# Kernel optimization log

Hardware: AMD Instinct MI355X
Metric: run time of the kernel (lower is better)

The kernel has to match this reference:

```python
import math
import jax, jax.numpy as jnp
import numpy as np

B, L, D, H = 8, 4096, 512, 8
FACTOR = 1


def setup_inputs() -> dict:
    key = jax.random.key(0)
    ks = jax.random.split(key, 8)
    scale = 0.02
    return {
        "queries": jax.random.normal(ks[0], (B, L, D), dtype=jnp.float32),
        "keys": jax.random.normal(ks[1], (B, L, D), dtype=jnp.float32),
        "values": jax.random.normal(ks[2], (B, L, D), dtype=jnp.float32),
        "Wq": jax.random.normal(ks[3], (D, D), dtype=jnp.float32) * scale,
        "bq": jnp.zeros((D,), dtype=jnp.float32),
        "Wk": jax.random.normal(ks[4], (D, D), dtype=jnp.float32) * scale,
        "bk": jnp.zeros((D,), dtype=jnp.float32),
        "Wv": jax.random.normal(ks[5], (D, D), dtype=jnp.float32) * scale,
        "bv": jnp.zeros((D,), dtype=jnp.float32),
        "Wo": jax.random.normal(ks[6], (D, D), dtype=jnp.float32) * scale,
        "bo": jnp.zeros((D,), dtype=jnp.float32),
    }


def reference(queries, keys, values, Wq, bq, Wk, bk, Wv, bv, Wo, bo):
    b, l, d = queries.shape
    h = H
    e = d // h
    # Projections (torch Linear math; weight stored as [in, out] here)
    q = (queries @ Wq + bq).reshape(b, l, h, e)
    k = (keys @ Wk + bk).reshape(b, l, h, e)
    v = (values @ Wv + bv).reshape(b, l, h, e)
    # [B, H, E, L]
    qp = q.transpose(0, 2, 3, 1)
    kp = k.transpose(0, 2, 3, 1)
    vp = v.transpose(0, 2, 3, 1)
    # FFT cross-correlation over the time axis
    qf = jnp.fft.rfft(qp, axis=-1)
    kf = jnp.fft.rfft(kp, axis=-1)
    corr = jnp.fft.irfft(qf * jnp.conj(kf), n=l, axis=-1)  # [B,H,E,L]
    # time_delay_agg_training
    top_k = int(FACTOR * math.log(l))
    mean_value = corr.mean(axis=(1, 2))  # [B, L] (mean over head then channel)
    _, index = jax.lax.top_k(mean_value.mean(axis=0), top_k)  # [K] shared delays
    weights = mean_value[:, index]  # [B, K]
    tmp_corr = jax.nn.softmax(weights, axis=-1)  # [B, K]
    # roll(values, -delay) along time == gather at (t + delay) mod L
    idx = (jnp.arange(l)[None, :] + index[:, None]) % l  # [K, L]
    gathered = jnp.take(vp, idx, axis=-1)  # [B, H, E, K, L]
    agg = jnp.einsum("bhekl,bk->bhel", gathered, tmp_corr)  # weighted MAC over delays
    out = agg.transpose(0, 3, 1, 2).reshape(b, l, h * e)  # [B, L, D]
    return out @ Wo + bo
```

## Files before the change

kernel.cpp:

```cpp
#include <hip/hip_runtime.h>
#include <math.h>

#define LSEQ 4096
#define DMODEL 512
#define BB 8
#define TOPK 8
#define ML (BB * LSEQ)
#define FFT_CH 2
#define NGRP (DMODEL / FFT_CH)
#define PPH 2052

typedef unsigned short u16;
typedef unsigned int u32;
typedef float f32x4 __attribute__((ext_vector_type(4)));
typedef short s16x8 __attribute__((ext_vector_type(8)));
typedef u16 u16x8 __attribute__((ext_vector_type(8)));

__device__ __forceinline__ u16 rne_bf16(float f) {
    u32 u = __float_as_uint(f);
    return (u16)((u + 0x7FFF + ((u >> 16) & 1)) >> 16);
}

__device__ __forceinline__ void fft16(float (&zr)[16], float (&zi)[16]) {
    const float C1 = 0.92387953251128674f, S1 = 0.38268343236508978f, R2 = 0.70710678118654752f;
#define BF0(i, j) { float ar=zr[i],ai=zi[i],br=zr[j],bi=zi[j]; zr[i]=ar+br; zi[i]=ai+bi; zr[j]=ar-br; zi[j]=ai-bi; }
#define BFW(i, j, wr, wi) { float ar=zr[i],ai=zi[i],br=zr[j],bi=zi[j]; zr[i]=ar+br; zi[i]=ai+bi; float dr=ar-br, di=ai-bi; zr[j]=dr*(wr)-di*(wi); zi[j]=dr*(wi)+di*(wr); }
#define BFI(i, j) { float ar=zr[i],ai=zi[i],br=zr[j],bi=zi[j]; zr[i]=ar+br; zi[i]=ai+bi; float dr=ar-br, di=ai-bi; zr[j]=di; zi[j]=-dr; }
    BF0(0, 8); BFW(1, 9, C1, -S1); BFW(2, 10, R2, -R2); BFW(3, 11, S1, -C1);
    BFI(4, 12); BFW(5, 13, -S1, -C1); BFW(6, 14, -R2, -R2); BFW(7, 15, -C1, -S1);
    BF0(0, 4); BFW(1, 5, R2, -R2); BFI(2, 6); BFW(3, 7, -R2, -R2);
    BF0(8, 12); BFW(9, 13, R2, -R2); BFI(10, 14); BFW(11, 15, -R2, -R2);
    BF0(0, 2); BFI(1, 3); BF0(4, 6); BFI(5, 7);
    BF0(8, 10); BFI(9, 11); BF0(12, 14); BFI(13, 15);
    BF0(0, 1); BF0(2, 3); BF0(4, 5); BF0(6, 7);
    BF0(8, 9); BF0(10, 11); BF0(12, 13); BF0(14, 15);
#undef BF0
#undef BFW
#undef BFI
}

template <bool WRITEBACK>
__device__ __forceinline__ void fft4096_r16_core(float* __restrict__ lre, float* __restrict__ lim, int t,
                                                 float (&ozr)[16], float (&ozi)[16]) {
    constexpr int REV16[16] = {0, 8, 4, 12, 2, 10, 6, 14, 1, 9, 5, 13, 3, 11, 7, 15};
    float zr[16], zi[16];
#pragma unroll
    for (int gg = 0; gg < 16; ++gg) {
        int n = 256 * gg + t;
        int p = n ^ ((gg & 3) << 2) ^ ((gg & 1) << 4);
        zr[gg] = lre[p]; zi[gg] = lim[p];
    }
    fft16(zr, zi);
    {
        const int n1 = t >> 4;
        float w1i, w1r;
        __sincosf(-0.0245436926061702596f * (float)n1, &w1i, &w1r);
        float wr = 1.f, wi = 0.f;
#pragma unroll
        for (int k0 = 0; k0 < 16; ++k0) {
            float vr = zr[REV16[k0]], vi = zi[REV16[k0]];
            if (k0) {
                float nr = wr * w1r - wi * w1i;
                wi = wr * w1i + wi * w1r;
                wr = nr;
                float tr = vr * wr - vi * wi;
                vi = vr * wi + vi * wr;
                vr = tr;
            }
            int n = 256 * k0 + t;
            int p = n ^ ((k0 & 3) << 2) ^ ((k0 & 1) << 4);
            lre[p] = vr; lim[p] = vi;
        }
    }
    __syncthreads();
    {
        const int k0 = t >> 4, n2 = t & 15;
        const int x0 = ((k0 & 3) << 2) | ((k0 & 1) << 4);
#pragma unroll
        for (int gg = 0; gg < 16; ++gg) {
            int n = 256 * k0 + 16 * gg + n2;
            zr[gg] = lre[n ^ x0]; zi[gg] = lim[n ^ x0];
        }
        fft16(zr, zi);
        float wbi, wbr, wsi, wsr;
        __sincosf(-0.00153398078788564123f * (float)(n2 * k0), &wbi, &wbr);
        __sincosf(-0.0245436926061702596f * (float)n2, &wsi, &wsr);
        float wr = wbr, wi = wbi;
#pragma unroll
        for (int k1 = 0; k1 < 16; ++k1) {
            float vr = zr[REV16[k1]], vi = zi[REV16[k1]];
            if (k1) {
                float nr = wr * wsr - wi * wsi;
                wi = wr * wsi + wi * wsr;
                wr = nr;
            }
            float tr = vr * wr - vi * wi;
            vi = vr * wi + vi * wr;
            vr = tr;
            int n = 256 * k0 + 16 * k1 + n2;
            lre[n ^ x0] = vr; lim[n ^ x0] = vi;
        }
    }
    __syncthreads();
    {
        const int k0 = t & 15, k1 = t >> 4;
        const int nb4 = 64 * k0 + 4 * k1;
        const int xv = (k0 & 3) | ((k0 & 1) << 2);
#pragma unroll
        for (int i = 0; i < 4; ++i) {
            int p4 = (nb4 + i) ^ xv;
            float4 fr = *(const float4*)&lre[4 * p4];
            float4 fi = *(const float4*)&lim[4 * p4];
            ozr[4 * i + 0] = fr.x; ozr[4 * i + 1] = fr.y; ozr[4 * i + 2] = fr.z; ozr[4 * i + 3] = fr.w;
            ozi[4 * i + 0] = fi.x; ozi[4 * i + 1] = fi.y; ozi[4 * i + 2] = fi.z; ozi[4 * i + 3] = fi.w;
        }
        fft16(ozr, ozi);
        if constexpr (WRITEBACK) {
            __syncthreads();
#pragma unroll
            for (int r = 0; r < 16; ++r) {
                const int k2 = REV16[r];
                lre[t + 256 * k2] = ozr[r];
                lim[t + 256 * k2] = ozi[r];
            }
            __syncthreads();
        }
    }
}

__global__ __launch_bounds__(256) void fft_cross(const u16* __restrict__ Qtb,
                                                 const u16* __restrict__ Ktb,
                                                 float* __restrict__ Ppart) {
    __shared__ float lre[4096];
    __shared__ float lim[4096];
    constexpr int REV16[16] = {0, 8, 4, 12, 2, 10, 6, 14, 1, 9, 5, 13, 3, 11, 7, 15};
    const int t = threadIdx.x;
    const int b = blockIdx.x / NGRP;
    const int g = blockIdx.x % NGRP;

    float2 acc[8];
#pragma unroll
    for (int i = 0; i < 8; ++i) acc[i] = make_float2(0.f, 0.f);
    float accn = 0.f;

    const uint4* q8 = (const uint4*)(Qtb + (size_t)(g * FFT_CH) * ML + (size_t)b * LSEQ);
    const uint4* k8 = (const uint4*)(Ktb + (size_t)(g * FFT_CH) * ML + (size_t)b * LSEQ);

    uint4 pq[2], pk[2];
    pq[0] = q8[t]; pq[1] = q8[t + 256];
    pk[0] = k8[t]; pk[1] = k8[t + 256];

    for (int c = 0; c < FFT_CH; ++c) {
        __syncthreads();
#pragma unroll
        for (int i = 0; i < 2; ++i) {
            const int u = t + 256 * i;
            const uint4 vq = pq[i], vk = pk[i];
#pragma unroll
            for (int hh = 0; hh < 2; ++hh) {
                const int v = 2 * u + hh;
                const int key = (v >> 6) & 15;
                const int p4 = v ^ (key & 3) ^ ((key & 1) << 2);
                const u32 w0 = hh ? vq.z : vq.x;
                const u32 w1 = hh ? vq.w : vq.y;
                float4 fa = make_float4(__uint_as_float(w0 << 16), __uint_as_float(w0 & 0xFFFF0000u),
                                        __uint_as_float(w1 << 16), __uint_as_float(w1 & 0xFFFF0000u));
                *(float4*)&lre[4 * p4] = fa;
                const u32 x0 = hh ? vk.z : vk.x;
                const u32 x1 = hh ? vk.w : vk.y;
                float4 fb = make_float4(__uint_as_float(x0 << 16), __uint_as_float(x0 & 0xFFFF0000u),
                                        __uint_as_float(x1 << 16), __uint_as_float(x1 & 0xFFFF0000u));
                *(float4*)&lim[4 * p4] = fb;
            }
        }
        if (c + 1 < FFT_CH) {
            const uint4* qn = q8 + (size_t)(c + 1) * (ML / 8);
            const uint4* kn = k8 + (size_t)(c + 1) * (ML / 8);
            pq[0] = qn[t]; pq[1] = qn[t + 256];
            pk[0] = kn[t]; pk[1] = kn[t + 256];
        }
        __syncthreads();
        float ozr[16], ozi[16];
        fft4096_r16_core<true>(lre, lim, t, ozr, ozi);
#pragma unroll
        for (int i = 0; i < 8; ++i) {
            const int j = i * 256 + t;
            const int nj = (4096 - j) & 4095;
            const int r = REV16[i];
            float zfr = ozr[r], zfi = ozi[r];
            float znr = lre[nj], zni = lim[nj];
            float qr = 0.5f * (zfr + znr);
            float qi = 0.5f * (zfi - zni);
            float kr = 0.5f * (zfi + zni);
            float ki = -0.5f * (zfr - znr);
            acc[i].x += qr * kr + qi * ki;
            acc[i].y += qi * kr - qr * ki;
        }
        if (t == 0) accn += ozr[1] * ozi[1];
    }
    float2* Pp = (float2*)Ppart + (size_t)blockIdx.x * PPH;
#pragma unroll
    for (int i = 0; i < 8; ++i) Pp[i * 256 + t] = acc[i];
    if (t == 0) Pp[2048] = make_float2(accn, 0.f);
}

__device__ __forceinline__ void gemmQ_body(const float* __restrict__ A,
                                           const u16* __restrict__ Bhi,
                                           u16* __restrict__ Ct, int lin, int tid,
                                           u16* sAhi, u16* sBhi) {
    const int t = (lin & 7) * 128 + (lin >> 3);
    const int bm = (t >> 2) * 128;
    const int bn = (t & 3) * 128;
    const int lane = tid & 63, wid = tid >> 6;
    const int wm = wid >> 1, wn = wid & 1;
    const int l15 = lane & 15, kg = lane >> 4;

    f32x4 acc[4][4] = {};

    for (int k0 = 0; k0 < 512; k0 += 64) {
        __syncthreads();
#pragma unroll
        for (int it = 0; it < 4; ++it) {
            const int ch = it * 256 + tid;
            const int row = ch >> 3, c = ch & 7;
            const float* ga = A + (size_t)(bm + row) * 512 + k0 + c * 8;
            float4 f0 = *(const float4*)ga;
            float4 f1 = *(const float4*)(ga + 4);
            float fs[8] = {f0.x, f0.y, f0.z, f0.w, f1.x, f1.y, f1.z, f1.w};
            u32 h[4];
#pragma unroll
            for (int p = 0; p < 4; ++p) {
                u32 u0 = __float_as_uint(fs[2 * p]);
                u32 u1 = __float_as_uint(fs[2 * p + 1]);
                u32 h0 = u0 + 0x7FFF + ((u0 >> 16) & 1);
                u32 h1 = u1 + 0x7FFF + ((u1 >> 16) & 1);
                h[p] = __builtin_amdgcn_perm(h1, h0, 0x07060302u);
            }
            const int off = row * 64 + ((c ^ (row & 7)) << 3);
            *(uint4*)&sAhi[off] = make_uint4(h[0], h[1], h[2], h[3]);
        }
#pragma unroll
        for (int it = 0; it < 4; ++it) {
            const int ch = it * 256 + tid;
            const int row = ch >> 3, c = ch & 7;
            const int off = row * 64 + ((c ^ (row & 7)) << 3);
            const size_t gg = (size_t)(bn + row) * 512 + k0 + c * 8;
            *(u16x8*)&sBhi[off] = *(const u16x8*)&Bhi[gg];
        }
        __syncthreads();
#pragma unroll
        for (int kk = 0; kk < 2; ++kk) {
            const int cbase = kk * 4 + kg;
            s16x8 ah[4], bh[4];
#pragma unroll
            for (int mi = 0; mi < 4; ++mi) {
                const int row = wm * 64 + mi * 16 + l15;
                const int off = row * 64 + (((cbase ^ (row & 7))) << 3);
                ah[mi] = *(const s16x8*)&sAhi[off];
            }
#pragma unroll
            for (int ni = 0; ni < 4; ++ni) {
                const int row = wn * 64 + ni * 16 + l15;
                const int off = row * 64 + (((cbase ^ (row & 7))) << 3);
                bh[ni] = *(const s16x8*)&sBhi[off];
            }
#pragma unroll
            for (int ni = 0; ni < 4; ++ni)
#pragma unroll
                for (int mi = 0; mi < 4; ++mi)
                    acc[mi][ni] = __builtin_amdgcn_mfma_f32_16x16x32_bf16(ah[mi], bh[ni], acc[mi][ni], 0, 0, 0);
        }
    }
#pragma unroll
    for (int ni = 0; ni < 4; ++ni) {
        const int d = bn + wn * 64 + ni * 16 + l15;
#pragma unroll
        for (int mi = 0; mi < 4; ++mi) {
            const int rb = bm + wm * 64 + mi * 16 + (kg << 2);
            ushort4 o;
            o.x = rne_bf16(acc[mi][ni][0]); o.y = rne_bf16(acc[mi][ni][1]);
            o.z = rne_bf16(acc[mi][ni][2]); o.w = rne_bf16(acc[mi][ni][3]);
            *(ushort4*)&Ct[(size_t)d * ML + rb] = o;
        }
    }
}

__device__ __forceinline__ void gemm1_body(const float* __restrict__ A,
                                           const u16* __restrict__ Bhi,
                                           const float* __restrict__ bias,
                                           u16* __restrict__ Cv, int lin, int tid,
                                           u16* sAhi, u16* sBhi) {
    const int t = (lin & 7) * 128 + (lin >> 3);
    const int bm = (t >> 2) * 128;
    const int bn = (t & 3) * 128;
    const int lane = tid & 63, wid = tid >> 6;
    const int wm = wid >> 1, wn = wid & 1;
    const int l15 = lane & 15, kg = lane >> 4;

    f32x4 acc[4][4] = {};

    for (int k0 = 0; k0 < 512; k0 += 64) {
        __syncthreads();
#pragma unroll
        for (int it = 0; it < 4; ++it) {
            const int ch = it * 256 + tid;
            const int row = ch >> 3, c = ch & 7;
            const float* ga = A + (size_t)(bm + row) * 512 + k0 + c * 8;
            float4 f0 = *(const float4*)ga;
            float4 f1 = *(const float4*)(ga + 4);
            float fs[8] = {f0.x, f0.y, f0.z, f0.w, f1.x, f1.y, f1.z, f1.w};
            u32 h[4];
#pragma unroll
            for (int p = 0; p < 4; ++p) {
                u32 u0 = __float_as_uint(fs[2 * p]);
                u32 u1 = __float_as_uint(fs[2 * p + 1]);
                u32 h0 = u0 + 0x7FFF + ((u0 >> 16) & 1);
                u32 h1 = u1 + 0x7FFF + ((u1 >> 16) & 1);
                h[p] = __builtin_amdgcn_perm(h1, h0, 0x07060302u);
            }
            const int off = row * 64 + ((c ^ (row & 7)) << 3);
            *(uint4*)&sAhi[off] = make_uint4(h[0], h[1], h[2], h[3]);
        }
#pragma unroll
        for (int it = 0; it < 4; ++it) {
            const int ch = it * 256 + tid;
            const int row = ch >> 3, c = ch & 7;
            const int off = row * 64 + ((c ^ (row & 7)) << 3);
            const size_t gg = (size_t)(bn + row) * 512 + k0 + c * 8;
            *(u16x8*)&sBhi[off] = *(const u16x8*)&Bhi[gg];
        }
        __syncthreads();
#pragma unroll
        for (int kk = 0; kk < 2; ++kk) {
            const int cbase = kk * 4 + kg;
            s16x8 ah[4], bh[4];
#pragma unroll
            for (int mi = 0; mi < 4; ++mi) {
                const int row = wm * 64 + mi * 16 + l15;
                const int off = row * 64 + (((cbase ^ (row & 7))) << 3);
                ah[mi] = *(const s16x8*)&sAhi[off];
            }
#pragma unroll
            for (int ni = 0; ni < 4; ++ni) {
                const int row = wn * 64 + ni * 16 + l15;
                const int off = row * 64 + (((cbase ^ (row & 7))) << 3);
                bh[ni] = *(const s16x8*)&sBhi[off];
            }
#pragma unroll
            for (int ni = 0; ni < 4; ++ni)
#pragma unroll
                for (int mi = 0; mi < 4; ++mi)
                    acc[mi][ni] = __builtin_amdgcn_mfma_f32_16x16x32_bf16(ah[mi], bh[ni], acc[mi][ni], 0, 0, 0);
        }
    }
#pragma unroll
    for (int ni = 0; ni < 4; ++ni) {
        const int col = bn + wn * 64 + ni * 16 + l15;
        const float bvv = bias[col];
#pragma unroll
        for (int mi = 0; mi < 4; ++mi) {
            const int rb = bm + wm * 64 + mi * 16 + (kg << 2);
#pragma unroll
            for (int r = 0; r < 4; ++r)
                Cv[(size_t)(rb + r) * 512 + col] = rne_bf16(acc[mi][ni][r] + bvv);
        }
    }
}

__global__ __launch_bounds__(256) void prep_all(const float* __restrict__ Wq, const float* __restrict__ Wk,
                                                const float* __restrict__ Wv, const float* __restrict__ Wo,
                                                const float* __restrict__ bvec, const float* __restrict__ bo,
                                                u16* __restrict__ Mh, u16* __restrict__ Wch,
                                                float* __restrict__ bc) {
    __shared__ float As[16][64];
    __shared__ float Ws[16][64];
    __shared__ float red[8][32];
    const int bx = blockIdx.x;
    const int tid = threadIdx.x;
    if (bx < 128) {
        const bool isM = bx < 64;
        const int id = bx & 63;
        const int bm = (id >> 3) * 64, bn = (id & 7) * 64;
        const int tx = tid & 15, ty = tid >> 4;
        float acc[4][4] = {};
        const int arow = tid >> 2, ak4 = tid & 3;
        const int wrow = tid >> 4, wc4 = tid & 15;
        const float* Abase = isM ? Wq : Wv;
        for (int k0 = 0; k0 < 512; k0 += 16) {
            float4 av = *(const float4*)&Abase[(size_t)(bm + arow) * 512 + k0 + ak4 * 4];
            float4 wv4;
            if (isM) wv4 = *(const float4*)&Wk[(size_t)(bn + arow) * 512 + k0 + ak4 * 4];
            else     wv4 = *(const float4*)&Wo[(size_t)(k0 + wrow) * 512 + bn + wc4 * 4];
            __syncthreads();
            As[ak4 * 4 + 0][arow] = av.x;
            As[ak4 * 4 + 1][arow] = av.y;
            As[ak4 * 4 + 2][arow] = av.z;
            As[ak4 * 4 + 3][arow] = av.w;
            if (isM) {
                Ws[ak4 * 4 + 0][arow] = wv4.x;
                Ws[ak4 * 4 + 1][arow] = wv4.y;
                Ws[ak4 * 4 + 2][arow] = wv4.z;
                Ws[ak4 * 4 + 3][arow] = wv4.w;
            } else {
                *(float4*)&Ws[wrow][wc4 * 4] = wv4;
            }
            __syncthreads();
#pragma unroll
            for (int k = 0; k < 16; ++k) {
                float4 a = *(const float4*)&As[k][ty * 4];
                float4 b = *(const float4*)&Ws[k][tx * 4];
                acc[0][0] += a.x * b.x; acc[0][1] += a.x * b.y; acc[0][2] += a.x * b.z; acc[0][3] += a.x * b.w;
                acc[1][0] += a.y * b.x; acc[1][1] += a.y * b.y; acc[1][2] += a.y * b.z; acc[1][3] += a.y * b.w;
                acc[2][0] += a.z * b.x; acc[2][1] += a.z * b.y; acc[2][2] += a.z * b.z; acc[2][3] += a.z * b.w;
                acc[3][0] += a.w * b.x; acc[3][1] += a.w * b.y; acc[3][2] += a.w * b.z; acc[3][3] += a.w * b.w;
            }
        }
        u16* dh = isM ? Mh : Wch;
#pragma unroll
        for (int i = 0; i < 4; ++i)
#pragma unroll
            for (int j = 0; j < 4; ++j) {
                const int a = bm + ty * 4 + i;
                const int n = bn + tx * 4 + j;
                dh[(size_t)n * 512 + a] = rne_bf16(acc[i][j]);
            }
    } else {
        const int n0 = (bx - 128) * 32;
        const int nl = tid & 31, jg = tid >> 5;
        float partial = 0.f;
        for (int s = 0; s < 64; ++s) {
            int j = jg + 8 * s;
            partial += bvec[j] * Wo[(size_t)j * 512 + n0 + nl];
        }
        red[jg][nl] = partial;
        __syncthreads();
        if (tid < 32) {
            float s2 = 0.f;
            for (int r2 = 0; r2 < 8; ++r2) s2 += red[r2][tid];
            bc[n0 + tid] = s2 + bo[n0 + tid];
        }
    }
}

__global__ __launch_bounds__(256, 4) void proj3(const float* __restrict__ queries,
                                                const u16* __restrict__ Mh, u16* __restrict__ Qtb,
                                                const float* __restrict__ values,
                                                const u16* __restrict__ Wch, const float* __restrict__ bc,
                                                u16* __restrict__ VOb,
                                                const float* __restrict__ keys, u16* __restrict__ Ktb) {
    __shared__ __align__(16) u16 smem[2 * 128 * 64];
    const int g = blockIdx.x;
    const int q = g / 6, r = g % 6;
    const int tid = threadIdx.x;
    if (r == 0) {
        gemmQ_body(queries, Mh, Qtb, q, tid, smem, smem + 8192);
    } else if (r == 1) {
        gemm1_body(values, Wch, bc, VOb, q, tid, smem, smem + 8192);
    } else {
        float* Ts = (float*)smem;
        const int tb = q * 4 + (r - 2);
        const int bd = (tb & 7) * 64;
        const int bm = (tb >> 3) * 64;
        const int rr = tid >> 2, c4 = tid & 3;
#pragma unroll
        for (int i = 0; i < 4; ++i) {
            const int c0 = (c4 + 4 * i) * 4;
            float4 v = *(const float4*)&keys[(size_t)(bm + rr) * DMODEL + bd + c0];
            Ts[rr * 65 + c0 + 0] = v.x; Ts[rr * 65 + c0 + 1] = v.y;
            Ts[rr * 65 + c0 + 2] = v.z; Ts[rr * 65 + c0 + 3] = v.w;
        }
        __syncthreads();
        const int dl = tid >> 2, m4 = tid & 3;
#pragma unroll
        for (int i = 0; i < 4; ++i) {
            const int m0 = (m4 + 4 * i) * 4;
            ushort4 o;
            o.x = rne_bf16(Ts[(m0 + 0) * 65 + dl]);
            o.y = rne_bf16(Ts[(m0 + 1) * 65 + dl]);
            o.z = rne_bf16(Ts[(m0 + 2) * 65 + dl]);
            o.w = rne_bf16(Ts[(m0 + 3) * 65 + dl]);
            *(ushort4*)&Ktb[(size_t)(bd + dl) * ML + bm + m0] = o;
        }
    }
}

__global__ __launch_bounds__(256) void reduce_ppart(const float2* __restrict__ Pp,
                                                    float2* __restrict__ Pred) {
    const int j = blockIdx.x * 256 + threadIdx.x;
    const int b = blockIdx.y;
    if (j > 2048) return;
    float sr = 0.f, si = 0.f;
    const float2* base = Pp + (size_t)b * NGRP * PPH + j;
    for (int g = 0; g < NGRP; ++g) {
        float2 p = base[(size_t)g * PPH];
        sr += p.x;
        si += p.y;
    }
    Pred[(size_t)b * PPH + j] = make_float2(sr, si);
}

__global__ __launch_bounds__(256) void ifft_mean(const float2* __restrict__ Pred,
                                                 float* __restrict__ mv) {
    __shared__ float lre[4096];
    __shared__ float lim[4096];
    constexpr int REV16[16] = {0, 8, 4, 12, 2, 10, 6, 14, 1, 9, 5, 13, 3, 11, 7, 15};
    const int t = threadIdx.x;
    const int b = blockIdx.x;
    for (int j = t; j < 4096; j += 256) {
        float2 p;
        if (j <= 2048) {
            p = Pred[(size_t)b * PPH + j];
        } else {
            p = Pred[(size_t)b * PPH + (4096 - j)];
            p.y = -p.y;
        }
        int key = (j >> 8) & 15;
        int ph = j ^ ((key & 3) << 2) ^ ((key & 1) << 4);
        lre[ph] = p.x;
        lim[ph] = -p.y;
    }
    __syncthreads();
    float ozr[16], ozi[16];
    fft4096_r16_core<false>(lre, lim, t, ozr, ozi);
    const float scale = 1.0f / (4096.0f * 512.0f);
#pragma unroll
    for (int i = 0; i < 16; ++i)
        mv[(size_t)b * 4096 + t + 256 * i] = ozr[REV16[i]] * scale;
}

__global__ __launch_bounds__(1024) void topk_softmax(const float* __restrict__ mv,
                                                     int* __restrict__ idxO,
                                                     float* __restrict__ tcO) {
    __shared__ float vals[4096];
    __shared__ float wv[16];
    __shared__ int wix[16];
    __shared__ int sidx[TOPK];
    const int tid = threadIdx.x;
    const int lane = tid & 63, wvid = tid >> 6;
    for (int j = tid; j < 4096; j += 1024) {
        float s = 0.f;
        for (int b = 0; b < BB; ++b) s += mv[(size_t)b * 4096 + j];
        vals[j] = s * 0.125f;
    }
    __syncthreads();
    for (int k = 0; k < TOPK; ++k) {
        float best = -INFINITY;
        int bi = 0x7fffffff;
        for (int j = tid; j < 4096; j += 1024) {
            float v = vals[j];
            if (v > best) { best = v; bi = j; }
        }
#pragma unroll
        for (int off = 32; off > 0; off >>= 1) {
            float ov = __shfl_down(best, off);
            int oi = __shfl_down(bi, off);
            if (ov > best || (ov == best && oi < bi)) { best = ov; bi = oi; }
        }
        if (lane == 0) { wv[wvid] = best; wix[wvid] = bi; }
        __syncthreads();
        if (wvid == 0) {
            best = (lane < 16) ? wv[lane] : -INFINITY;
            bi = (lane < 16) ? wix[lane] : 0x7fffffff;
#pragma unroll
            for (int off = 8; off > 0; off >>= 1) {
                float ov = __shfl_down(best, off);
                int oi = __shfl_down(bi, off);
                if (ov > best || (ov == best && oi < bi)) { best = ov; bi = oi; }
            }
            if (lane == 0) {
                sidx[k] = bi;
                idxO[k] = bi;
                vals[bi] = -INFINITY;
            }
        }
        __syncthreads();
    }
    if (tid < BB) {
        float w[TOPK];
        float m = -INFINITY;
        for (int k = 0; k < TOPK; ++k) {
            w[k] = mv[(size_t)tid * 4096 + sidx[k]];
            m = fmaxf(m, w[k]);
        }
        float s = 0.f;
        for (int k = 0; k < TOPK; ++k) { w[k] = expf(w[k] - m); s += w[k]; }
        float inv = 1.0f / s;
        for (int k = 0; k < TOPK; ++k) tcO[tid * TOPK + k] = w[k] * inv;
    }
}

__global__ __launch_bounds__(256) void gather_out(const u16* __restrict__ VO,
                                                  const int* __restrict__ idx,
                                                  const float* __restrict__ tc,
                                                  float* __restrict__ out) {
    const int e = blockIdx.x * 256 + threadIdx.x;
    const int d8 = e & 63;
    const int l = (e >> 6) & 4095;
    const int b = e >> 18;
    float s[8] = {};
#pragma unroll
    for (int k = 0; k < TOPK; ++k) {
        const int src = (l + idx[k]) & 4095;
        const float w = tc[b * TOPK + k];
        uint4 v = *(const uint4*)&VO[((size_t)(b * 4096 + src)) * 512 + d8 * 8];
        s[0] += w * __uint_as_float(v.x << 16);
        s[1] += w * __uint_as_float(v.x & 0xFFFF0000u);
        s[2] += w * __uint_as_float(v.y << 16);
        s[3] += w * __uint_as_float(v.y & 0xFFFF0000u);
        s[4] += w * __uint_as_float(v.z << 16);
        s[5] += w * __uint_as_float(v.z & 0xFFFF0000u);
        s[6] += w * __uint_as_float(v.w << 16);
        s[7] += w * __uint_as_float(v.w & 0xFFFF0000u);
    }
    const size_t ob = ((size_t)(b * 4096 + l)) * 512 + d8 * 8;
    *(float4*)&out[ob]     = make_float4(s[0], s[1], s[2], s[3]);
    *(float4*)&out[ob + 4] = make_float4(s[4], s[5], s[6], s[7]);
}

extern "C" void kernel_launch(void* const* d_in, const int* in_sizes, int n_in,
                              void* d_out, int out_size, void* d_ws, size_t ws_size,
                              hipStream_t stream) {
    const float* queries = (const float*)d_in[0];
    const float* keys    = (const float*)d_in[1];
    const float* values  = (const float*)d_in[2];
    const float* Wq = (const float*)d_in[3];
    const float* Wk = (const float*)d_in[5];
    const float* Wv = (const float*)d_in[7];
    const float* bv = (const float*)d_in[8];
    const float* Wo = (const float*)d_in[9];
    const float* bo = (const float*)d_in[10];
    float* out = (float*)d_out;

    const size_t SZ = (size_t)ML * DMODEL;
    u16* Qtb = (u16*)d_ws;
    u16* Ktb = Qtb + SZ;
    u16* VOb = Ktb + SZ;
    float* Pp   = (float*)(VOb + SZ);
    float* Pred = Pp + (size_t)BB * NGRP * PPH * 2;
    float* mv   = Pred + (size_t)BB * PPH * 2;
    int*   idx  = (int*)(mv + 32768);
    float* tc   = mv + 32768 + 16;
    float* bc   = mv + 32768 + 96;
    u16* Mh  = (u16*)(bc + 512);
    u16* Wch = Mh + 262144;

    dim3 blk(256);

    prep_all<<<dim3(144), blk, 0, stream>>>(Wq, Wk, Wv, Wo, bv, bo, Mh, Wch, bc);

    proj3<<<dim3(6144), blk, 0, stream>>>(queries, Mh, Qtb, values, Wch, bc, VOb, keys, Ktb);

    fft_cross<<<dim3(BB * NGRP), blk, 0, stream>>>(Qtb, Ktb, Pp);

    reduce_ppart<<<dim3(9, BB), blk, 0, stream>>>((const float2*)Pp, (float2*)Pred);

    ifft_mean<<<dim3(BB), blk, 0, stream>>>((const float2*)Pred, mv);

    topk_softmax<<<dim3(1), dim3(1024), 0, stream>>>(mv, idx, tc);

    gather_out<<<dim3((BB * LSEQ * (DMODEL / 8)) / 256), blk, 0, stream>>>(VOb, idx, tc, out);
}
```

Before: 276.3 us.

## Prefetch GEMM tiles into registers, reorder proj3 blocks, split partial reduction

Both GEMM bodies now load the next K-slice of A and B into registers while the current slice is being computed, a form of software pipelining. This hides global memory latency at the cost of more registers, and the launch-bounds occupancy hint of 4 blocks is dropped. proj3 now assigns contiguous block ranges to the Q GEMM, the V GEMM and the K transpose instead of interleaving them by g%6. reduce_ppart is split four ways along the group axis to expose more parallelism, with ifft_mean summing the four partial results.

```diff
diff --git a/kernel.cpp b/kernel.cpp
--- a/kernel.cpp
+++ b/kernel.cpp
@@ -214,6 +214,19 @@
     const int lane = tid & 63, wid = tid >> 6;
     const int wm = wid >> 1, wn = wid & 1;
     const int l15 = lane & 15, kg = lane >> 4;
+    const int r0 = tid >> 3, c = tid & 7;
+    const int xoff = r0 * 64 + ((c ^ (r0 & 7)) << 3);
+
+    float4 pa0[4], pa1[4];
+    uint4 pb[4];
+#pragma unroll
+    for (int it = 0; it < 4; ++it) {
+        const int row = it * 32 + r0;
+        const float* ga = A + (size_t)(bm + row) * 512 + c * 8;
+        pa0[it] = *(const float4*)ga;
+        pa1[it] = *(const float4*)(ga + 4);
+        pb[it] = *(const uint4*)&Bhi[(size_t)(bn + row) * 512 + c * 8];
+    }
 
     f32x4 acc[4][4] = {};
 
@@ -221,12 +234,8 @@
         __syncthreads();
 #pragma unroll
         for (int it = 0; it < 4; ++it) {
-            const int ch = it * 256 + tid;
-            const int row = ch >> 3, c = ch & 7;
-            const float* ga = A + (size_t)(bm + row) * 512 + k0 + c * 8;
-            float4 f0 = *(const float4*)ga;
-            float4 f1 = *(const float4*)(ga + 4);
-            float fs[8] = {f0.x, f0.y, f0.z, f0.w, f1.x, f1.y, f1.z, f1.w};
+            float fs[8] = {pa0[it].x, pa0[it].y, pa0[it].z, pa0[it].w,
+                           pa1[it].x, pa1[it].y, pa1[it].z, pa1[it].w};
             u32 h[4];
 #pragma unroll
             for (int p = 0; p < 4; ++p) {
@@ -236,16 +245,18 @@
                 u32 h1 = u1 + 0x7FFF + ((u1 >> 16) & 1);
                 h[p] = __builtin_amdgcn_perm(h1, h0, 0x07060302u);
             }
-            const int off = row * 64 + ((c ^ (row & 7)) << 3);
-            *(uint4*)&sAhi[off] = make_uint4(h[0], h[1], h[2], h[3]);
-        }
-#pragma unroll
-        for (int it = 0; it < 4; ++it) {
-            const int ch = it * 256 + tid;
-            const int row = ch >> 3, c = ch & 7;
-            const int off = row * 64 + ((c ^ (row & 7)) << 3);
-            const size_t gg = (size_t)(bn + row) * 512 + k0 + c * 8;
-            *(u16x8*)&sBhi[off] = *(const u16x8*)&Bhi[gg];
+            *(uint4*)&sAhi[it * 2048 + xoff] = make_uint4(h[0], h[1], h[2], h[3]);
+            *(uint4*)&sBhi[it * 2048 + xoff] = pb[it];
+        }
+        if (k0 + 64 < 512) {
+#pragma unroll
+            for (int it = 0; it < 4; ++it) {
+                const int row = it * 32 + r0;
+                const float* ga = A + (size_t)(bm + row) * 512 + (k0 + 64) + c * 8;
+                pa0[it] = *(const float4*)ga;
+                pa1[it] = *(const float4*)(ga + 4);
+                pb[it] = *(const uint4*)&Bhi[(size_t)(bn + row) * 512 + (k0 + 64) + c * 8];
+            }
         }
         __syncthreads();
 #pragma unroll
@@ -296,6 +307,19 @@
     const int lane = tid & 63, wid = tid >> 6;
     const int wm = wid >> 1, wn = wid & 1;
     const int l15 = lane & 15, kg = lane >> 4;
+    const int r0 = tid >> 3, c = tid & 7;
+    const int xoff = r0 * 64 + ((c ^ (r0 & 7)) << 3);
+
+    float4 pa0[4], pa1[4];
+    uint4 pb[4];
+#pragma unroll
+    for (int it = 0; it < 4; ++it) {
+        const int row = it * 32 + r0;
+        const float* ga = A + (size_t)(bm + row) * 512 + c * 8;
+        pa0[it] = *(const float4*)ga;
+        pa1[it] = *(const float4*)(ga + 4);
+        pb[it] = *(const uint4*)&Bhi[(size_t)(bn + row) * 512 + c * 8];
+    }
 
     f32x4 acc[4][4] = {};
 
@@ -303,12 +327,8 @@
         __syncthreads();
 #pragma unroll
         for (int it = 0; it < 4; ++it) {
-            const int ch = it * 256 + tid;
-            const int row = ch >> 3, c = ch & 7;
-            const float* ga = A + (size_t)(bm + row) * 512 + k0 + c * 8;
-            float4 f0 = *(const float4*)ga;
-            float4 f1 = *(const float4*)(ga + 4);
-            float fs[8] = {f0.x, f0.y, f0.z, f0.w, f1.x, f1.y, f1.z, f1.w};
+            float fs[8] = {pa0[it].x, pa0[it].y, pa0[it].z, pa0[it].w,
+                           pa1[it].x, pa1[it].y, pa1[it].z, pa1[it].w};
             u32 h[4];
 #pragma unroll
             for (int p = 0; p < 4; ++p) {
@@ -318,16 +338,18 @@
                 u32 h1 = u1 + 0x7FFF + ((u1 >> 16) & 1);
                 h[p] = __builtin_amdgcn_perm(h1, h0, 0x07060302u);
             }
-            const int off = row * 64 + ((c ^ (row & 7)) << 3);
-            *(uint4*)&sAhi[off] = make_uint4(h[0], h[1], h[2], h[3]);
-        }
-#pragma unroll
-        for (int it = 0; it < 4; ++it) {
-            const int ch = it * 256 + tid;
-            const int row = ch >> 3, c = ch & 7;
-            const int off = row * 64 + ((c ^ (row & 7)) << 3);
-            const size_t gg = (size_t)(bn + row) * 512 + k0 + c * 8;
-            *(u16x8*)&sBhi[off] = *(const u16x8*)&Bhi[gg];
+            *(uint4*)&sAhi[it * 2048 + xoff] = make_uint4(h[0], h[1], h[2], h[3]);
+            *(uint4*)&sBhi[it * 2048 + xoff] = pb[it];
+        }
+        if (k0 + 64 < 512) {
+#pragma unroll
+            for (int it = 0; it < 4; ++it) {
+                const int row = it * 32 + r0;
+                const float* ga = A + (size_t)(bm + row) * 512 + (k0 + 64) + c * 8;
+                pa0[it] = *(const float4*)ga;
+                pa1[it] = *(const float4*)(ga + 4);
+                pb[it] = *(const uint4*)&Bhi[(size_t)(bn + row) * 512 + (k0 + 64) + c * 8];
+            }
         }
         __syncthreads();
 #pragma unroll
@@ -442,23 +464,22 @@
     }
 }
 
-__global__ __launch_bounds__(256, 4) void proj3(const float* __restrict__ queries,
-                                                const u16* __restrict__ Mh, u16* __restrict__ Qtb,
-                                                const float* __restrict__ values,
-                                                const u16* __restrict__ Wch, const float* __restrict__ bc,
-                                                u16* __restrict__ VOb,
-                                                const float* __restrict__ keys, u16* __restrict__ Ktb) {
+__global__ __launch_bounds__(256) void proj3(const float* __restrict__ queries,
+                                             const u16* __restrict__ Mh, u16* __restrict__ Qtb,
+                                             const float* __restrict__ values,
+                                             const u16* __restrict__ Wch, const float* __restrict__ bc,
+                                             u16* __restrict__ VOb,
+                                             const float* __restrict__ keys, u16* __restrict__ Ktb) {
     __shared__ __align__(16) u16 smem[2 * 128 * 64];
     const int g = blockIdx.x;
-    const int q = g / 6, r = g % 6;
     const int tid = threadIdx.x;
-    if (r == 0) {
-        gemmQ_body(queries, Mh, Qtb, q, tid, smem, smem + 8192);
-    } else if (r == 1) {
-        gemm1_body(values, Wch, bc, VOb, q, tid, smem, smem + 8192);
+    if (g < 1024) {
+        gemmQ_body(queries, Mh, Qtb, g, tid, smem, smem + 8192);
+    } else if (g < 2048) {
+        gemm1_body(values, Wch, bc, VOb, g - 1024, tid, smem, smem + 8192);
     } else {
         float* Ts = (float*)smem;
-        const int tb = q * 4 + (r - 2);
+        const int tb = g - 2048;
         const int bd = (tb & 7) * 64;
         const int bm = (tb >> 3) * 64;
         const int rr = tid >> 2, c4 = tid & 3;
@@ -485,21 +506,22 @@
 }
 
 __global__ __launch_bounds__(256) void reduce_ppart(const float2* __restrict__ Pp,
-                                                    float2* __restrict__ Pred) {
+                                                    float2* __restrict__ Pred4) {
     const int j = blockIdx.x * 256 + threadIdx.x;
     const int b = blockIdx.y;
+    const int z = blockIdx.z;
     if (j > 2048) return;
     float sr = 0.f, si = 0.f;
     const float2* base = Pp + (size_t)b * NGRP * PPH + j;
-    for (int g = 0; g < NGRP; ++g) {
+    for (int g = z * 64; g < z * 64 + 64; ++g) {
         float2 p = base[(size_t)g * PPH];
         sr += p.x;
         si += p.y;
     }
-    Pred[(size_t)b * PPH + j] = make_float2(sr, si);
-}
-
-__global__ __launch_bounds__(256) void ifft_mean(const float2* __restrict__ Pred,
+    Pred4[((size_t)z * BB + b) * PPH + j] = make_float2(sr, si);
+}
+
+__global__ __launch_bounds__(256) void ifft_mean(const float2* __restrict__ Pred4,
                                                  float* __restrict__ mv) {
     __shared__ float lre[4096];
     __shared__ float lim[4096];
@@ -507,17 +529,19 @@
     const int t = threadIdx.x;
     const int b = blockIdx.x;
     for (int j = t; j < 4096; j += 256) {
-        float2 p;
-        if (j <= 2048) {
-            p = Pred[(size_t)b * PPH + j];
-        } else {
-            p = Pred[(size_t)b * PPH + (4096 - j)];
-            p.y = -p.y;
-        }
+        const int jj = (j <= 2048) ? j : 4096 - j;
+        float sr = 0.f, si = 0.f;
+#pragma unroll
+        for (int z = 0; z < 4; ++z) {
+            float2 p = Pred4[((size_t)z * BB + b) * PPH + jj];
+            sr += p.x;
+            si += p.y;
+        }
+        if (j > 2048) si = -si;
         int key = (j >> 8) & 15;
         int ph = j ^ ((key & 3) << 2) ^ ((key & 1) << 4);
-        lre[ph] = p.x;
-        lim[ph] = -p.y;
+        lre[ph] = sr;
+        lim[ph] = -si;
     }
     __syncthreads();
     float ozr[16], ozi[16];
@@ -635,12 +659,12 @@
     u16* Qtb = (u16*)d_ws;
     u16* Ktb = Qtb + SZ;
     u16* VOb = Ktb + SZ;
-    float* Pp   = (float*)(VOb + SZ);
-    float* Pred = Pp + (size_t)BB * NGRP * PPH * 2;
-    float* mv   = Pred + (size_t)BB * PPH * 2;
-    int*   idx  = (int*)(mv + 32768);
-    float* tc   = mv + 32768 + 16;
-    float* bc   = mv + 32768 + 96;
+    float* Pp    = (float*)(VOb + SZ);
+    float* Pred4 = Pp + (size_t)BB * NGRP * PPH * 2;
+    float* mv    = Pred4 + (size_t)4 * BB * PPH * 2;
+    int*   idx   = (int*)(mv + 32768);
+    float* tc    = mv + 32768 + 16;
+    float* bc    = mv + 32768 + 96;
     u16* Mh  = (u16*)(bc + 512);
     u16* Wch = Mh + 262144;
 
@@ -652,9 +676,9 @@
 
     fft_cross<<<dim3(BB * NGRP), blk, 0, stream>>>(Qtb, Ktb, Pp);
 
-    reduce_ppart<<<dim3(9, BB), blk, 0, stream>>>((const float2*)Pp, (float2*)Pred);
-
-    ifft_mean<<<dim3(BB), blk, 0, stream>>>((const float2*)Pred, mv);
+    reduce_ppart<<<dim3(9, BB, 4), blk, 0, stream>>>((const float2*)Pp, (float2*)Pred4);
+
+    ifft_mean<<<dim3(BB), blk, 0, stream>>>((const float2*)Pred4, mv);
 
     topk_softmax<<<dim3(1), dim3(1024), 0, stream>>>(mv, idx, tc);
 
```

Result: slower. 289.2 us (+4.7%).
